# Optimization experiments

Hardware: AMD Instinct MI355X
Metric: run time of the kernel (lower is better)

The kernel has to match this reference:

```python
import jax, jax.numpy as jnp
import numpy as np

D_MODEL = 256
D_ENERGY = 128
TEMP = 0.07

def _lin_init(key, fan_in, fan_out):
    k1, k2 = jax.random.split(key)
    bound = 1.0 / np.sqrt(fan_in)
    W = jax.random.uniform(k1, (fan_out, fan_in), jnp.float32, -bound, bound)
    b = jax.random.uniform(k2, (fan_out,), jnp.float32, -bound, bound)
    return W, b

def setup_inputs() -> dict:
    key = jax.random.key(0)
    ks = jax.random.split(key, 8)
    B, NNEG = 32768, 16
    anchor = jax.random.normal(ks[0], (B, D_MODEL), jnp.float32)
    positive = jax.random.normal(ks[1], (B, D_MODEL), jnp.float32)
    negatives = jax.random.normal(ks[2], (B, NNEG, D_MODEL), jnp.float32)
    # joint_encoder: Linear(512,256) -> GELU -> Linear(256,128) -> GELU (dropout = identity in eval)
    W1, b1 = _lin_init(ks[3], 2 * D_MODEL, 2 * D_ENERGY)
    W2, b2 = _lin_init(ks[4], 2 * D_ENERGY, D_ENERGY)
    # energy_head: Linear(128,64) -> GELU -> Linear(64,1)
    W3, b3 = _lin_init(ks[5], D_ENERGY, D_ENERGY // 2)
    W4, b4 = _lin_init(ks[6], D_ENERGY // 2, 1)
    return {"anchor": anchor, "positive": positive, "negatives": negatives,
            "W1": W1, "b1": b1, "W2": W2, "b2": b2, "W3": W3, "b3": b3, "W4": W4, "b4": b4}

def _energy(x, y, W1, b1, W2, b2, W3, b3, W4, b4):
    # x, y: (..., d_model). Returns energy (...,). Exact (erf) GELU to match torch nn.GELU.
    joint = jnp.concatenate([x, y], axis=-1)                      # (..., 2*d_model)
    h = jax.nn.gelu(joint @ W1.T + b1, approximate=False)          # (..., 2*d_energy)
    h = jax.nn.gelu(h @ W2.T + b2, approximate=False)              # (..., d_energy)
    h = jax.nn.gelu(h @ W3.T + b3, approximate=False)              # (..., d_energy//2)
    return (h @ W4.T + b4)[..., 0]                                 # (...,)

def reference(anchor, positive, negatives, W1, b1, W2, b2, W3, b3, W4, b4):
    B, NNEG, D = negatives.shape
    # Batch positive + all negatives into one fused pass: ys (B, 1+NNEG, D)
    ys = jnp.concatenate([positive[:, None, :], negatives], axis=1)
    xs = jnp.broadcast_to(anchor[:, None, :], (B, 1 + NNEG, D))
    all_energies = _energy(xs, ys, W1, b1, W2, b2, W3, b3, W4, b4)  # (B, 1+NNEG)
    logits = -all_energies / TEMP
    # cross entropy with label 0
    loss = jnp.mean(jax.nn.logsumexp(logits, axis=1) - logits[:, 0])
    pos_energy = jnp.mean(all_energies[:, 0])
    neg_energy = jnp.mean(all_energies[:, 1:])
    accuracy = jnp.mean((jnp.argmin(all_energies, axis=1) == 0).astype(jnp.float32))
    return loss, pos_energy, neg_energy, accuracy
```

## Files before the change

kernel.cpp:

```cpp
#include <hip/hip_runtime.h>
#include <math.h>


#define NROWS 32768
#define NC 17
#define NPAIRS (NROWS * NC)
#define INV_T (1.0f / 0.07f)

using bf16x8 = __attribute__((ext_vector_type(8))) short;
using f32x4  = __attribute__((ext_vector_type(4))) float;

#define PK_W1A 0
#define PK_W1Y 65536
#define PK_W2  131072
#define PK_W3  163840
#define APRE_OFF_BYTES 344064
#define EN_OFF_BYTES   (344064 + (size_t)NROWS * 256 * 4)

__device__ inline unsigned short f2b(float f) {
  union { float f; unsigned u; } v; v.f = f;
  return (unsigned short)((v.u + 0x7FFFu + ((v.u >> 16) & 1u)) >> 16);
}
__device__ inline unsigned f2b2(float a, float b) {
#if __has_builtin(__builtin_amdgcn_cvt_pk_bf16_f32)
  typedef __attribute__((ext_vector_type(2))) short s2;
  union { s2 s; unsigned u; } v; v.s = __builtin_amdgcn_cvt_pk_bf16_f32(a, b);
  return v.u;
#else
  return (unsigned)f2b(a) | ((unsigned)f2b(b) << 16);
#endif
}
__device__ inline float b2f(unsigned short b) {
  union { unsigned u; float f; } v; v.u = ((unsigned)b) << 16; return v.f;
}
__device__ inline float gelu_f(float x) {
  float x2 = x * x;
  float w  = x * fmaf(x2, 0.07135837f, 1.59576912f);
  float t  = w * -1.44269504f;
#if __has_builtin(__builtin_amdgcn_exp2f)
  float e  = __builtin_amdgcn_exp2f(t);
#else
  float e  = exp2f(t);
#endif
  return x * __builtin_amdgcn_rcpf(1.0f + e);
}

__global__ void zero_k(float* out) {
  if (threadIdx.x < 4) out[threadIdx.x] = 0.0f;
}

__global__ void pack_w(const float* __restrict__ W1, const float* __restrict__ W2,
                       const float* __restrict__ W3, unsigned short* __restrict__ pk) {
  int gid = blockIdx.x * 256 + threadIdx.x;
  int tile = gid >> 6, lane = gid & 63;
  const float* W; int NT, ld, koff, lt; unsigned short* dst;
  if (tile < 128)      { W = W1; NT = 16; ld = 512; koff = 0;   lt = tile;       dst = pk + PK_W1A; }
  else if (tile < 256) { W = W1; NT = 16; ld = 512; koff = 256; lt = tile - 128; dst = pk + PK_W1Y; }
  else if (tile < 320) { W = W2; NT = 8;  ld = 256; koff = 0;   lt = tile - 256; dst = pk + PK_W2;  }
  else                 { W = W3; NT = 4;  ld = 128; koff = 0;   lt = tile - 320; dst = pk + PK_W3;  }
  int kt = lt / NT, nt = lt - kt * NT;
  int k = kt * 32 + (lane >> 4) * 8;
  int n = nt * 16 + (lane & 15);
  const float* src = W + (size_t)n * ld + koff + k;
  unsigned short o[8];
#pragma unroll
  for (int j = 0; j < 8; ++j) o[j] = f2b(src[j]);
  ushort4* d = (ushort4*)(dst + ((size_t)lt * 64 + lane) * 8);
  d[0] = make_ushort4(o[0], o[1], o[2], o[3]);
  d[1] = make_ushort4(o[4], o[5], o[6], o[7]);
}

__global__ __launch_bounds__(256) void apre_k(const float* __restrict__ anchor,
                                              const float* __restrict__ b1,
                                              const unsigned short* __restrict__ pk,
                                              float* __restrict__ apre) {
  __shared__ __align__(16) unsigned short bufA[64 * 264];
  int t = threadIdx.x;
  int m0 = blockIdx.x * 64;
  for (int it = 0; it < 16; ++it) {
    int e = (it * 256 + t) * 4;
    int m = e >> 8, k = e & 255;
    float4 v = *(const float4*)(anchor + (size_t)(m0 + m) * 256 + k);
    *(uint2*)&bufA[m * 264 + k] = make_uint2(f2b2(v.x, v.y), f2b2(v.z, v.w));
  }
  __syncthreads();
  int wave = t >> 6, lane = t & 63, quad = lane >> 4, lid = lane & 15;
  f32x4 acc[4][4];
#pragma unroll
  for (int i = 0; i < 4; ++i)
#pragma unroll
    for (int j = 0; j < 4; ++j) { acc[i][j][0]=0.f; acc[i][j][1]=0.f; acc[i][j][2]=0.f; acc[i][j][3]=0.f; }
  const bf16x8* Wb = (const bf16x8*)(pk + PK_W1A);
  for (int kt = 0; kt < 8; ++kt) {
    bf16x8 a[4], b[4];
#pragma unroll
    for (int mt = 0; mt < 4; ++mt)
      a[mt] = *(const bf16x8*)&bufA[(mt * 16 + lid) * 264 + kt * 32 + quad * 8];
#pragma unroll
    for (int nt = 0; nt < 4; ++nt)
      b[nt] = Wb[(size_t)(kt * 16 + wave * 4 + nt) * 64 + lane];
#pragma unroll
    for (int mt = 0; mt < 4; ++mt)
#pragma unroll
      for (int nt = 0; nt < 4; ++nt)
        acc[mt][nt] = __builtin_amdgcn_mfma_f32_16x16x32_bf16(a[mt], b[nt], acc[mt][nt], 0, 0, 0);
  }
#pragma unroll
  for (int mt = 0; mt < 4; ++mt)
#pragma unroll
    for (int nt = 0; nt < 4; ++nt) {
      int n = wave * 64 + nt * 16 + lid;
      float bias = b1[n];
#pragma unroll
      for (int r = 0; r < 4; ++r) {
        int m = mt * 16 + quad * 4 + r;
        apre[(size_t)(m0 + m) * 256 + n] = acc[mt][nt][r] + bias;
      }
    }
}

__global__ __launch_bounds__(256) void fused_k(const float* __restrict__ positive,
                                               const float* __restrict__ negatives,
                                               const float* __restrict__ apre,
                                               const unsigned short* __restrict__ pk,
                                               const float* __restrict__ b2v,
                                               const float* __restrict__ b3v,
                                               const float* __restrict__ W4,
                                               const float* __restrict__ b4v,
                                               float* __restrict__ energies) {
  __shared__ __align__(16) unsigned short bufA[64 * 264];
  __shared__ __align__(16) unsigned char bufCmem[64 * 136 * 2];
  unsigned short* bufC = (unsigned short*)bufCmem;
  float* apre_s = (float*)bufCmem;
  int t = threadIdx.x;
  int p0 = blockIdx.x * 64;
  int r0 = p0 / 17;
  int rN = (p0 + 63) / 17 - r0 + 1;
  for (int i = t; i < rN * 256; i += 256)
    apre_s[i] = apre[(size_t)(r0 + (i >> 8)) * 256 + (i & 255)];
  for (int it = 0; it < 16; ++it) {
    int e = (it * 256 + t) * 4;
    int m = e >> 8, k = e & 255;
    int p = p0 + m;
    int r = p / 17, c = p - r * 17;
    const float* src = (c == 0) ? (positive + (size_t)r * 256)
                                : (negatives + ((size_t)r * 16 + (c - 1)) * 256);
    float4 v = *(const float4*)(src + k);
    *(uint2*)&bufA[m * 264 + k] = make_uint2(f2b2(v.x, v.y), f2b2(v.z, v.w));
  }
  __syncthreads();
  int wave = t >> 6, lane = t & 63, quad = lane >> 4, lid = lane & 15;

  f32x4 acc[4][4];
#pragma unroll
  for (int i = 0; i < 4; ++i)
#pragma unroll
    for (int j = 0; j < 4; ++j) { acc[i][j][0]=0.f; acc[i][j][1]=0.f; acc[i][j][2]=0.f; acc[i][j][3]=0.f; }
  {
    const bf16x8* Wb = (const bf16x8*)(pk + PK_W1Y);
    for (int kt = 0; kt < 8; ++kt) {
      bf16x8 a[4], b[4];
#pragma unroll
      for (int mt = 0; mt < 4; ++mt)
        a[mt] = *(const bf16x8*)&bufA[(mt * 16 + lid) * 264 + kt * 32 + quad * 8];
#pragma unroll
      for (int nt = 0; nt < 4; ++nt)
        b[nt] = Wb[(size_t)(kt * 16 + wave * 4 + nt) * 64 + lane];
#pragma unroll
      for (int mt = 0; mt < 4; ++mt)
#pragma unroll
        for (int nt = 0; nt < 4; ++nt)
          acc[mt][nt] = __builtin_amdgcn_mfma_f32_16x16x32_bf16(a[mt], b[nt], acc[mt][nt], 0, 0, 0);
    }
  }
  __syncthreads();
#pragma unroll
  for (int mt = 0; mt < 4; ++mt) {
    int ri[4];
#pragma unroll
    for (int r = 0; r < 4; ++r)
      ri[r] = (p0 + mt * 16 + quad * 4 + r) / 17 - r0;
#pragma unroll
    for (int nt = 0; nt < 4; ++nt) {
      int n = wave * 64 + nt * 16 + lid;
#pragma unroll
      for (int r = 0; r < 4; ++r) {
        int m = mt * 16 + quad * 4 + r;
        float val = acc[mt][nt][r] + apre_s[ri[r] * 256 + n];
        bufA[m * 264 + n] = f2b(gelu_f(val));
      }
    }
  }
  __syncthreads();

  f32x4 acc2[4][2];
#pragma unroll
  for (int i = 0; i < 4; ++i)
#pragma unroll
    for (int j = 0; j < 2; ++j) { acc2[i][j][0]=0.f; acc2[i][j][1]=0.f; acc2[i][j][2]=0.f; acc2[i][j][3]=0.f; }
  {
    const bf16x8* Wb = (const bf16x8*)(pk + PK_W2);
    for (int kt = 0; kt < 8; ++kt) {
      bf16x8 a[4], b[2];
#pragma unroll
      for (int mt = 0; mt < 4; ++mt)
        a[mt] = *(const bf16x8*)&bufA[(mt * 16 + lid) * 264 + kt * 32 + quad * 8];
#pragma unroll
      for (int nt = 0; nt < 2; ++nt)
        b[nt] = Wb[(size_t)(kt * 8 + wave * 2 + nt) * 64 + lane];
#pragma unroll
      for (int mt = 0; mt < 4; ++mt)
#pragma unroll
        for (int nt = 0; nt < 2; ++nt)
          acc2[mt][nt] = __builtin_amdgcn_mfma_f32_16x16x32_bf16(a[mt], b[nt], acc2[mt][nt], 0, 0, 0);
    }
  }
#pragma unroll
  for (int mt = 0; mt < 4; ++mt)
#pragma unroll
    for (int nt = 0; nt < 2; ++nt) {
      int n = wave * 32 + nt * 16 + lid;
      float bias = b2v[n];
#pragma unroll
      for (int r = 0; r < 4; ++r) {
        int m = mt * 16 + quad * 4 + r;
        bufC[m * 136 + n] = f2b(gelu_f(acc2[mt][nt][r] + bias));
      }
    }
  __syncthreads();

  f32x4 acc3[4];
#pragma unroll
  for (int i = 0; i < 4; ++i) { acc3[i][0]=0.f; acc3[i][1]=0.f; acc3[i][2]=0.f; acc3[i][3]=0.f; }
  {
    const bf16x8* Wb = (const bf16x8*)(pk + PK_W3);
    for (int kt = 0; kt < 4; ++kt) {
      bf16x8 a[4];
#pragma unroll
      for (int mt = 0; mt < 4; ++mt)
        a[mt] = *(const bf16x8*)&bufC[(mt * 16 + lid) * 136 + kt * 32 + quad * 8];
      bf16x8 b = Wb[(size_t)(kt * 4 + wave) * 64 + lane];
#pragma unroll
      for (int mt = 0; mt < 4; ++mt)
        acc3[mt] = __builtin_amdgcn_mfma_f32_16x16x32_bf16(a[mt], b, acc3[mt], 0, 0, 0);
    }
  }
  {
    int n = wave * 16 + lid;
    float bias = b3v[n];
#pragma unroll
    for (int mt = 0; mt < 4; ++mt)
#pragma unroll
      for (int r = 0; r < 4; ++r) {
        int m = mt * 16 + quad * 4 + r;
        bufA[m * 72 + n] = f2b(gelu_f(acc3[mt][r] + bias));
      }
  }
  __syncthreads();

  if (t < 64) {
    float s = b4v[0];
#pragma unroll
    for (int kk = 0; kk < 64; ++kk) s += b2f(bufA[t * 72 + kk]) * W4[kk];
    energies[p0 + t] = s;
  }
}

__global__ __launch_bounds__(256) void reduce_k(const float* __restrict__ E,
                                                float* __restrict__ out) {
  __shared__ float sd[256];
  int r = blockIdx.x * 256 + threadIdx.x;
  const float* ep = E + (size_t)r * 17;
  float e[17];
#pragma unroll
  for (int i = 0; i < 17; ++i) e[i] = ep[i];
  float li[17];
#pragma unroll
  for (int i = 0; i < 17; ++i) li[i] = -e[i] * INV_T;
  float lmax = li[0];
#pragma unroll
  for (int i = 1; i < 17; ++i) lmax = fmaxf(lmax, li[i]);
  float se = 0.f;
#pragma unroll
  for (int i = 0; i < 17; ++i) se += expf(li[i] - lmax);
  float loss_t = (logf(se) + lmax) - li[0];
  float posv = e[0];
  float negv = 0.f;
#pragma unroll
  for (int i = 1; i < 17; ++i) negv += e[i];
  int mi = 0; float mv = e[0];
#pragma unroll
  for (int i = 1; i < 17; ++i) if (e[i] < mv) { mv = e[i]; mi = i; }
  float accv = (mi == 0) ? 1.f : 0.f;

  float vals[4] = { loss_t, posv, negv, accv };
  const float scales[4] = { 1.0f / NROWS, 1.0f / NROWS, 1.0f / (NROWS * 16.0f), 1.0f / NROWS };
#pragma unroll
  for (int j = 0; j < 4; ++j) {
    sd[threadIdx.x] = vals[j];
    __syncthreads();
    for (int s = 128; s > 0; s >>= 1) {
      if (threadIdx.x < s) sd[threadIdx.x] += sd[threadIdx.x + s];
      __syncthreads();
    }
    if (threadIdx.x == 0) atomicAdd(out + j, sd[0] * scales[j]);
    __syncthreads();
  }
}

extern "C" void kernel_launch(void* const* d_in, const int* in_sizes, int n_in,
                              void* d_out, int out_size, void* d_ws, size_t ws_size,
                              hipStream_t stream) {
  (void)in_sizes; (void)n_in; (void)out_size; (void)ws_size;
  const float* anchor    = (const float*)d_in[0];
  const float* positive  = (const float*)d_in[1];
  const float* negatives = (const float*)d_in[2];
  const float* W1 = (const float*)d_in[3];
  const float* b1 = (const float*)d_in[4];
  const float* W2 = (const float*)d_in[5];
  const float* b2 = (const float*)d_in[6];
  const float* W3 = (const float*)d_in[7];
  const float* b3 = (const float*)d_in[8];
  const float* W4 = (const float*)d_in[9];
  const float* b4 = (const float*)d_in[10];
  float* out = (float*)d_out;
  unsigned short* pk = (unsigned short*)d_ws;
  float* apre = (float*)((char*)d_ws + APRE_OFF_BYTES);
  float* energies = (float*)((char*)d_ws + EN_OFF_BYTES);

  hipLaunchKernelGGL(zero_k, dim3(1), dim3(64), 0, stream, out);
  hipLaunchKernelGGL(pack_w, dim3(84), dim3(256), 0, stream, W1, W2, W3, pk);
  hipLaunchKernelGGL(apre_k, dim3(512), dim3(256), 0, stream, anchor, b1, pk, apre);
  hipLaunchKernelGGL(fused_k, dim3(8704), dim3(256), 0, stream,
                     positive, negatives, apre, pk, b2, b3, W4, b4, energies);
  hipLaunchKernelGGL(reduce_k, dim3(128), dim3(256), 0, stream, energies, out);
}
```

Before: 867.3 us.

## Halve fused block tile to 32 pairs and fold biases and final dot into MFMA epilogues

The fused MLP kernel now handles 32 pairs per block instead of 64. This halves shared memory and accumulator registers, and a launch bound of 6 blocks per CU asks for higher occupancy. Biases and the precomputed anchor projection seed the MFMA accumulators directly, GELU outputs are packed two at a time into bf16, and the last 64-wide dot product with W4 is done with wave shuffles instead of a serial 64-step loop on one wave. The grid doubles, so per-block setup and weight fetches from L2 are repeated more often, and MFMA work per weight load is lower.

```diff
diff --git a/kernel.cpp b/kernel.cpp
--- a/kernel.cpp
+++ b/kernel.cpp
@@ -119,26 +119,25 @@
     }
 }
 
-__global__ __launch_bounds__(256) void fused_k(const float* __restrict__ positive,
-                                               const float* __restrict__ negatives,
-                                               const float* __restrict__ apre,
-                                               const unsigned short* __restrict__ pk,
-                                               const float* __restrict__ b2v,
-                                               const float* __restrict__ b3v,
-                                               const float* __restrict__ W4,
-                                               const float* __restrict__ b4v,
-                                               float* __restrict__ energies) {
-  __shared__ __align__(16) unsigned short bufA[64 * 264];
-  __shared__ __align__(16) unsigned char bufCmem[64 * 136 * 2];
-  unsigned short* bufC = (unsigned short*)bufCmem;
-  float* apre_s = (float*)bufCmem;
+__global__ __launch_bounds__(256, 6) void fused_k(const float* __restrict__ positive,
+                                                  const float* __restrict__ negatives,
+                                                  const float* __restrict__ apre,
+                                                  const unsigned short* __restrict__ pk,
+                                                  const float* __restrict__ b2v,
+                                                  const float* __restrict__ b3v,
+                                                  const float* __restrict__ W4,
+                                                  const float* __restrict__ b4v,
+                                                  float* __restrict__ energies) {
+  __shared__ __align__(16) unsigned short bufA[32 * 264];
+  __shared__ __align__(16) float apre_s[3 * 256];
   int t = threadIdx.x;
-  int p0 = blockIdx.x * 64;
+  int p0 = blockIdx.x * 32;
   int r0 = p0 / 17;
-  int rN = (p0 + 63) / 17 - r0 + 1;
+  int rN = (p0 + 31) / 17 - r0 + 1;
   for (int i = t; i < rN * 256; i += 256)
     apre_s[i] = apre[(size_t)(r0 + (i >> 8)) * 256 + (i & 255)];
-  for (int it = 0; it < 16; ++it) {
+#pragma unroll
+  for (int it = 0; it < 8; ++it) {
     int e = (it * 256 + t) * 4;
     int m = e >> 8, k = e & 255;
     int p = p0 + m;
@@ -151,23 +150,35 @@
   __syncthreads();
   int wave = t >> 6, lane = t & 63, quad = lane >> 4, lid = lane & 15;
 
-  f32x4 acc[4][4];
-#pragma unroll
-  for (int i = 0; i < 4; ++i)
-#pragma unroll
-    for (int j = 0; j < 4; ++j) { acc[i][j][0]=0.f; acc[i][j][1]=0.f; acc[i][j][2]=0.f; acc[i][j][3]=0.f; }
+  f32x4 acc[2][4];
+  {
+    int ri0[4], ri1[4];
+#pragma unroll
+    for (int r = 0; r < 4; ++r) ri0[r] = (p0 + quad * 4 + r) / 17 - r0;
+#pragma unroll
+    for (int r = 0; r < 4; ++r) ri1[r] = (p0 + 16 + quad * 4 + r) / 17 - r0;
+#pragma unroll
+    for (int nt = 0; nt < 4; ++nt) {
+      int n = wave * 64 + nt * 16 + lid;
+#pragma unroll
+      for (int r = 0; r < 4; ++r) {
+        acc[0][nt][r] = apre_s[ri0[r] * 256 + n];
+        acc[1][nt][r] = apre_s[ri1[r] * 256 + n];
+      }
+    }
+  }
   {
     const bf16x8* Wb = (const bf16x8*)(pk + PK_W1Y);
     for (int kt = 0; kt < 8; ++kt) {
-      bf16x8 a[4], b[4];
-#pragma unroll
-      for (int mt = 0; mt < 4; ++mt)
+      bf16x8 a[2], b[4];
+#pragma unroll
+      for (int mt = 0; mt < 2; ++mt)
         a[mt] = *(const bf16x8*)&bufA[(mt * 16 + lid) * 264 + kt * 32 + quad * 8];
 #pragma unroll
       for (int nt = 0; nt < 4; ++nt)
         b[nt] = Wb[(size_t)(kt * 16 + wave * 4 + nt) * 64 + lane];
 #pragma unroll
-      for (int mt = 0; mt < 4; ++mt)
+      for (int mt = 0; mt < 2; ++mt)
 #pragma unroll
         for (int nt = 0; nt < 4; ++nt)
           acc[mt][nt] = __builtin_amdgcn_mfma_f32_16x16x32_bf16(a[mt], b[nt], acc[mt][nt], 0, 0, 0);
@@ -175,94 +186,106 @@
   }
   __syncthreads();
 #pragma unroll
-  for (int mt = 0; mt < 4; ++mt) {
-    int ri[4];
-#pragma unroll
-    for (int r = 0; r < 4; ++r)
-      ri[r] = (p0 + mt * 16 + quad * 4 + r) / 17 - r0;
+  for (int mt = 0; mt < 2; ++mt)
 #pragma unroll
     for (int nt = 0; nt < 4; ++nt) {
       int n = wave * 64 + nt * 16 + lid;
-#pragma unroll
-      for (int r = 0; r < 4; ++r) {
-        int m = mt * 16 + quad * 4 + r;
-        float val = acc[mt][nt][r] + apre_s[ri[r] * 256 + n];
-        bufA[m * 264 + n] = f2b(gelu_f(val));
-      }
-    }
-  }
-  __syncthreads();
-
-  f32x4 acc2[4][2];
-#pragma unroll
-  for (int i = 0; i < 4; ++i)
-#pragma unroll
-    for (int j = 0; j < 2; ++j) { acc2[i][j][0]=0.f; acc2[i][j][1]=0.f; acc2[i][j][2]=0.f; acc2[i][j][3]=0.f; }
+      int mb = mt * 16 + quad * 4;
+      unsigned u01 = f2b2(gelu_f(acc[mt][nt][0]), gelu_f(acc[mt][nt][1]));
+      unsigned u23 = f2b2(gelu_f(acc[mt][nt][2]), gelu_f(acc[mt][nt][3]));
+      bufA[(mb + 0) * 264 + n] = (unsigned short)u01;
+      bufA[(mb + 1) * 264 + n] = (unsigned short)(u01 >> 16);
+      bufA[(mb + 2) * 264 + n] = (unsigned short)u23;
+      bufA[(mb + 3) * 264 + n] = (unsigned short)(u23 >> 16);
+    }
+  __syncthreads();
+
+  f32x4 acc2[2][2];
+  {
+#pragma unroll
+    for (int nt = 0; nt < 2; ++nt) {
+      float bb = b2v[wave * 32 + nt * 16 + lid];
+#pragma unroll
+      for (int mt = 0; mt < 2; ++mt)
+#pragma unroll
+        for (int r = 0; r < 4; ++r) acc2[mt][nt][r] = bb;
+    }
+  }
   {
     const bf16x8* Wb = (const bf16x8*)(pk + PK_W2);
     for (int kt = 0; kt < 8; ++kt) {
-      bf16x8 a[4], b[2];
-#pragma unroll
-      for (int mt = 0; mt < 4; ++mt)
+      bf16x8 a[2], b[2];
+#pragma unroll
+      for (int mt = 0; mt < 2; ++mt)
         a[mt] = *(const bf16x8*)&bufA[(mt * 16 + lid) * 264 + kt * 32 + quad * 8];
 #pragma unroll
       for (int nt = 0; nt < 2; ++nt)
         b[nt] = Wb[(size_t)(kt * 8 + wave * 2 + nt) * 64 + lane];
 #pragma unroll
-      for (int mt = 0; mt < 4; ++mt)
+      for (int mt = 0; mt < 2; ++mt)
 #pragma unroll
         for (int nt = 0; nt < 2; ++nt)
           acc2[mt][nt] = __builtin_amdgcn_mfma_f32_16x16x32_bf16(a[mt], b[nt], acc2[mt][nt], 0, 0, 0);
     }
   }
-#pragma unroll
-  for (int mt = 0; mt < 4; ++mt)
+  __syncthreads();
+  unsigned short* bufC = bufA;
+#pragma unroll
+  for (int mt = 0; mt < 2; ++mt)
 #pragma unroll
     for (int nt = 0; nt < 2; ++nt) {
       int n = wave * 32 + nt * 16 + lid;
-      float bias = b2v[n];
-#pragma unroll
-      for (int r = 0; r < 4; ++r) {
-        int m = mt * 16 + quad * 4 + r;
-        bufC[m * 136 + n] = f2b(gelu_f(acc2[mt][nt][r] + bias));
-      }
-    }
-  __syncthreads();
-
-  f32x4 acc3[4];
-#pragma unroll
-  for (int i = 0; i < 4; ++i) { acc3[i][0]=0.f; acc3[i][1]=0.f; acc3[i][2]=0.f; acc3[i][3]=0.f; }
+      int mb = mt * 16 + quad * 4;
+      unsigned u01 = f2b2(gelu_f(acc2[mt][nt][0]), gelu_f(acc2[mt][nt][1]));
+      unsigned u23 = f2b2(gelu_f(acc2[mt][nt][2]), gelu_f(acc2[mt][nt][3]));
+      bufC[(mb + 0) * 136 + n] = (unsigned short)u01;
+      bufC[(mb + 1) * 136 + n] = (unsigned short)(u01 >> 16);
+      bufC[(mb + 2) * 136 + n] = (unsigned short)u23;
+      bufC[(mb + 3) * 136 + n] = (unsigned short)(u23 >> 16);
+    }
+  __syncthreads();
+
+  f32x4 acc3[2];
+  {
+    float bb = b3v[wave * 16 + lid];
+#pragma unroll
+    for (int mt = 0; mt < 2; ++mt)
+#pragma unroll
+      for (int r = 0; r < 4; ++r) acc3[mt][r] = bb;
+  }
   {
     const bf16x8* Wb = (const bf16x8*)(pk + PK_W3);
     for (int kt = 0; kt < 4; ++kt) {
-      bf16x8 a[4];
-#pragma unroll
-      for (int mt = 0; mt < 4; ++mt)
+      bf16x8 a[2];
+#pragma unroll
+      for (int mt = 0; mt < 2; ++mt)
         a[mt] = *(const bf16x8*)&bufC[(mt * 16 + lid) * 136 + kt * 32 + quad * 8];
       bf16x8 b = Wb[(size_t)(kt * 4 + wave) * 64 + lane];
 #pragma unroll
-      for (int mt = 0; mt < 4; ++mt)
+      for (int mt = 0; mt < 2; ++mt)
         acc3[mt] = __builtin_amdgcn_mfma_f32_16x16x32_bf16(a[mt], b, acc3[mt], 0, 0, 0);
     }
   }
   {
-    int n = wave * 16 + lid;
-    float bias = b3v[n];
-#pragma unroll
-    for (int mt = 0; mt < 4; ++mt)
+    float w4n = W4[wave * 16 + lid];
+    float* epart = apre_s;
+#pragma unroll
+    for (int mt = 0; mt < 2; ++mt)
 #pragma unroll
       for (int r = 0; r < 4; ++r) {
-        int m = mt * 16 + quad * 4 + r;
-        bufA[m * 72 + n] = f2b(gelu_f(acc3[mt][r] + bias));
+        float v = gelu_f(acc3[mt][r]) * w4n;
+        v += __shfl_xor(v, 1);
+        v += __shfl_xor(v, 2);
+        v += __shfl_xor(v, 4);
+        v += __shfl_xor(v, 8);
+        if (lid == 0) epart[(mt * 16 + quad * 4 + r) * 4 + wave] = v;
       }
   }
   __syncthreads();
-
-  if (t < 64) {
-    float s = b4v[0];
-#pragma unroll
-    for (int kk = 0; kk < 64; ++kk) s += b2f(bufA[t * 72 + kk]) * W4[kk];
-    energies[p0 + t] = s;
+  if (t < 32) {
+    const float* epart = apre_s;
+    energies[p0 + t] = b4v[0] + epart[t * 4 + 0] + epart[t * 4 + 1]
+                     + epart[t * 4 + 2] + epart[t * 4 + 3];
   }
 }
 
@@ -331,7 +354,7 @@
   hipLaunchKernelGGL(zero_k, dim3(1), dim3(64), 0, stream, out);
   hipLaunchKernelGGL(pack_w, dim3(84), dim3(256), 0, stream, W1, W2, W3, pk);
   hipLaunchKernelGGL(apre_k, dim3(512), dim3(256), 0, stream, anchor, b1, pk, apre);
-  hipLaunchKernelGGL(fused_k, dim3(8704), dim3(256), 0, stream,
+  hipLaunchKernelGGL(fused_k, dim3(NPAIRS / 32), dim3(256), 0, stream,
                      positive, negatives, apre, pk, b2, b3, W4, b4, energies);
   hipLaunchKernelGGL(reduce_k, dim3(128), dim3(256), 0, stream, energies, out);
 }
```

After: 860.1 us. No clear change (-0.8%).
